# Optimization experiments

Hardware: AMD Instinct MI355X
Metric: run time of the kernel (lower is better)

The kernel has to match this reference:

```python
import jax, jax.numpy as jnp
import numpy as np

B = 1
DIM = 128
NUM_HEADS = 8
HEAD_DIM = DIM // NUM_HEADS
RES = (4, 16, 16, 16)            # (L, D, H, W)
FINE = (2, 8, 8, 8)
COARSE = (1, 2, 2, 2)
FINE_STRIDE = tuple(r // f for r, f in zip(RES, FINE))      # (2,2,2,2)
COARSE_STRIDE = tuple(r // c for r, c in zip(RES, COARSE))  # (4,8,8,8)
LOCAL = (1, 2, 2, 2)
HIDDEN = 512
SCALE = HEAD_DIM ** -0.5
EPS = 1e-5
_DN = jax.lax.ConvDimensionNumbers((0, 1, 2, 3, 4, 5), (0, 1, 2, 3, 4, 5), (0, 1, 2, 3, 4, 5))


def conv4d(x, w, b, stride=(1, 1, 1, 1)):
    # x: (B, L, C, D, H, W); channel axis is 2 (matches repo Conv4d usage). 'same'-style k//2 pad.
    xc = jnp.transpose(x, (0, 2, 1, 3, 4, 5))  # B,C,L,D,H,W
    pads = [(k // 2, k // 2) for k in w.shape[2:]]
    y = jax.lax.conv_general_dilated(xc, w, window_strides=stride, padding=pads, dimension_numbers=_DN)
    y = y + b[None, :, None, None, None, None]
    return jnp.transpose(y, (0, 2, 1, 3, 4, 5))


def layernorm(x, w, b):
    mu = jnp.mean(x, -1, keepdims=True)
    var = jnp.mean(jnp.square(x - mu), -1, keepdims=True)
    return (x - mu) * jax.lax.rsqrt(var + EPS) * w + b


def cnorm(x, w, b):
    # LayerNorm over channel axis (axis 2) of (B,L,C,D,H,W)
    xt = jnp.transpose(x, (0, 1, 3, 4, 5, 2))
    xt = layernorm(xt, w, b)
    return jnp.transpose(xt, (0, 1, 5, 2, 3, 4))


def to_tokens(t):
    # (B,L,C,D,H,W) -> (B, L*D*H*W, C)
    b, c = t.shape[0], t.shape[2]
    return jnp.swapaxes(jnp.transpose(t, (0, 2, 1, 3, 4, 5)).reshape(b, c, -1), 1, 2)


def split_heads(t):
    b, n, c = t.shape
    return jnp.transpose(t.reshape(b, n, NUM_HEADS, c // NUM_HEADS), (0, 2, 1, 3))


def slg(x, q_w, q_b, k_w, k_b, v_w, v_b, p_w, p_b, f_w, f_b, c_w, c_b, ln_w, ln_b):
    Bx, L, C, D, H, W = x.shape
    N = L * D * H * W
    q = split_heads(to_tokens(conv4d(x, q_w, q_b)))          # (B,h,N,hd)
    xc = conv4d(x, c_w, c_b, COARSE_STRIDE)                  # coarse pyramid (B,1,C,2,2,2)
    xf = conv4d(x, f_w, f_b, FINE_STRIDE)                    # fine pyramid   (B,2,C,8,8,8)
    kc = to_tokens(conv4d(xc, k_w, k_b))
    kf = to_tokens(conv4d(xf, k_w, k_b))
    vc = to_tokens(conv4d(xc, v_w, v_b))
    vf = to_tokens(conv4d(xf, v_w, v_b))
    k = split_heads(layernorm(jnp.concatenate([kc, kf], 1), ln_w, ln_b))
    v = split_heads(layernorm(jnp.concatenate([vc, vf], 1), ln_w, ln_b))
    attn = jax.nn.softmax(jnp.einsum('bhqd,bhkd->bhqk', q, k) * SCALE, axis=-1)
    y = jnp.einsum('bhqk,bhkd->bhqd', attn, v)               # (B,h,N,hd)
    y = jnp.transpose(y, (0, 2, 1, 3)).reshape(Bx, N, C)
    y = jnp.swapaxes(jnp.swapaxes(y, 1, 2).reshape(Bx, C, L, D, H, W), 1, 2)
    return conv4d(y, p_w, p_b)


def _win(t):
    # (B,Lh,C,D,H,W) -> (B, n_windows, heads, win_tokens, hd)
    b, l, c, d, h, w = t.shape
    ll, ld, lh, lw = LOCAL
    nl, nd, nh, nw = l // ll, d // ld, h // lh, w // lw
    t = jnp.transpose(t, (0, 2, 1, 3, 4, 5)).reshape(b, c, nl, ll, nd, ld, nh, lh, nw, lw)
    t = jnp.transpose(t, (0, 2, 4, 6, 8, 3, 5, 7, 9, 1))
    t = t.reshape(b, nl * nd * nh * nw, ll * ld * lh * lw, NUM_HEADS, c // NUM_HEADS)
    return jnp.transpose(t, (0, 1, 3, 2, 4))


def _unwin(y, shape):
    b, l, c, d, h, w = shape
    ll, ld, lh, lw = LOCAL
    nl, nd, nh, nw = l // ll, d // ld, h // lh, w // lw
    y = jnp.transpose(y, (0, 1, 3, 2, 4)).reshape(b, nl, nd, nh, nw, ll, ld, lh, lw, c)
    y = jnp.transpose(y, (0, 9, 1, 5, 2, 6, 3, 7, 4, 8)).reshape(b, c, l, d, h, w)
    return jnp.swapaxes(y, 1, 2)


def tlg(x, q_w, q_b, k_w, k_b, v_w, v_b, p_w, p_b):
    # stage < 2: first temporal half cross-attends with second half (windowed)
    L = x.shape[1]
    xs, xe = x[:, :L // 2], x[:, L // 2:]

    def cross(xq, xkv):
        q = _win(conv4d(xq, q_w, q_b))
        k = _win(conv4d(xkv, k_w, k_b))
        v = _win(conv4d(xkv, v_w, v_b))
        a = jax.nn.softmax(jnp.einsum('bnhqd,bnhkd->bnhqk', q, k) * SCALE, axis=-1)
        y = _unwin(jnp.einsum('bnhqk,bnhkd->bnhqd', a, v), xq.shape)
        return conv4d(y, p_w, p_b)

    return jnp.concatenate([cross(xs, xe), cross(xe, xs)], axis=1)


def _forward(x, n1_w, n1_b, tq_w, tq_b, tk_w, tk_b, tv_w, tv_b, tp_w, tp_b,
             n2_w, n2_b, sq_w, sq_b, sk_w, sk_b, sv_w, sv_b, sp_w, sp_b,
             sf_w, sf_b, sc_w, sc_b, sn_w, sn_b,
             n3_w, n3_b, m1_w, m1_b, m2_w, m2_b):
    x = x + tlg(cnorm(x, n1_w, n1_b), tq_w, tq_b, tk_w, tk_b, tv_w, tv_b, tp_w, tp_b)
    x = x + slg(cnorm(x, n2_w, n2_b), sq_w, sq_b, sk_w, sk_b, sv_w, sv_b, sp_w, sp_b,
                sf_w, sf_b, sc_w, sc_b, sn_w, sn_b)
    x = x + conv4d(jax.nn.relu(conv4d(cnorm(x, n3_w, n3_b), m1_w, m1_b)), m2_w, m2_b)
    return x


def setup_inputs():
    keys = iter(jax.random.split(jax.random.key(0), 64))

    def rn(shape, s=0.02):
        return jax.random.normal(next(keys), shape, dtype=jnp.float32) * s

    L, D, H, W = RES
    inp = {"x": jax.random.normal(next(keys), (B, L, DIM, D, H, W), dtype=jnp.float32)}
    for n in ("n1", "n2", "n3", "sn"):
        inp[n + "_w"] = jnp.ones((DIM,), jnp.float32)
        inp[n + "_b"] = jnp.zeros((DIM,), jnp.float32)
    for n in ("tq", "tk", "tv", "tp"):
        inp[n + "_w"] = rn((DIM, DIM, 3, 1, 1, 1))
        inp[n + "_b"] = jnp.zeros((DIM,), jnp.float32)
    for n in ("sq", "sk", "sv", "sp", "sf", "sc"):
        inp[n + "_w"] = rn((DIM, DIM, 1, 3, 3, 3))
        inp[n + "_b"] = jnp.zeros((DIM,), jnp.float32)
    inp["m1_w"] = rn((HIDDEN, DIM, 3, 3, 3, 3))
    inp["m1_b"] = jnp.zeros((HIDDEN,), jnp.float32)
    inp["m2_w"] = rn((DIM, HIDDEN, 3, 3, 3, 3))
    inp["m2_b"] = jnp.zeros((DIM,), jnp.float32)
    return inp


def reference(x, n1_w, n1_b, n2_w, n2_b, n3_w, n3_b, sn_w, sn_b,
              tq_w, tq_b, tk_w, tk_b, tv_w, tv_b, tp_w, tp_b,
              sq_w, sq_b, sk_w, sk_b, sv_w, sv_b, sp_w, sp_b,
              sf_w, sf_b, sc_w, sc_b, m1_w, m1_b, m2_w, m2_b):
    return _forward(x, n1_w, n1_b, tq_w, tq_b, tk_w, tk_b, tv_w, tv_b, tp_w, tp_b,
                    n2_w, n2_b, sq_w, sq_b, sk_w, sk_b, sv_w, sv_b, sp_w, sp_b,
                    sf_w, sf_b, sc_w, sc_b, sn_w, sn_b,
                    n3_w, n3_b, m1_w, m1_b, m2_w, m2_b)
```

## Files before the change

### kernel.cpp

```cpp
#include <hip/hip_runtime.h>

typedef unsigned short u16;
typedef __attribute__((ext_vector_type(8))) short bf16x8;
typedef __attribute__((ext_vector_type(4))) float f32x4;

#define PITCH 40

__device__ __forceinline__ u16 f2bf(float f) {
  union { float f; unsigned u; } v; v.f = f;
  unsigned r = v.u + 0x7fffu + ((v.u >> 16) & 1u);
  return (u16)(r >> 16);
}
__device__ __forceinline__ float bf2f(u16 h) {
  union { unsigned u; float f; } v; v.u = ((unsigned)h) << 16;
  return v.f;
}
__device__ __forceinline__ float4 load4bf(const u16* p) {
  ushort4 h = *(const ushort4*)p;
  return make_float4(bf2f(h.x), bf2f(h.y), bf2f(h.z), bf2f(h.w));
}
__device__ __forceinline__ void gll16(const u16* g, u16* l) {
  __builtin_amdgcn_global_load_lds(
      (const __attribute__((address_space(1))) unsigned int*)g,
      (__attribute__((address_space(3))) unsigned int*)l, 16, 0, 0);
}

__global__ __launch_bounds__(256) void k_tin(const float* __restrict__ x,
                                             float* __restrict__ xt) {
  __shared__ float t[32][33];
  int s0 = blockIdx.x * 32, c0 = blockIdx.y * 32, l = blockIdx.z;
  int r = threadIdx.x >> 3, q4 = (threadIdx.x & 7) * 4;
  float4 v = *(const float4*)(x + ((long)(l * 128 + c0 + r) << 12) + s0 + q4);
  t[r][q4] = v.x; t[r][q4 + 1] = v.y; t[r][q4 + 2] = v.z; t[r][q4 + 3] = v.w;
  __syncthreads();
  float4 o = {t[q4][r], t[q4 + 1][r], t[q4 + 2][r], t[q4 + 3][r]};
  *(float4*)(xt + ((long)(l * 4096 + s0 + r) << 7) + c0 + q4) = o;
}

__global__ __launch_bounds__(256) void k_tout(const float* __restrict__ xt,
                                              float* __restrict__ out) {
  __shared__ float t[32][33];
  int s0 = blockIdx.x * 32, c0 = blockIdx.y * 32, l = blockIdx.z;
  int r = threadIdx.x >> 3, q4 = (threadIdx.x & 7) * 4;
  float4 v = *(const float4*)(xt + ((long)(l * 4096 + s0 + r) << 7) + c0 + q4);
  t[r][q4] = v.x; t[r][q4 + 1] = v.y; t[r][q4 + 2] = v.z; t[r][q4 + 3] = v.w;
  __syncthreads();
  float4 o = {t[q4][r], t[q4 + 1][r], t[q4 + 2][r], t[q4 + 3][r]};
  *(float4*)(out + ((long)(l * 128 + c0 + r) << 12) + s0 + q4) = o;
}

__global__ __launch_bounds__(256) void k_zeropage(u16* __restrict__ zp) {
  zp[threadIdx.x] = 0; zp[threadIdx.x + 256] = 0;
  zp[threadIdx.x + 512] = 0; zp[threadIdx.x + 768] = 0;
}

__global__ __launch_bounds__(256) void k_ln_f2b(const float* __restrict__ X,
                                                const float* __restrict__ g,
                                                const float* __restrict__ b,
                                                u16* __restrict__ Y, int M,
                                                u16* __restrict__ Y2, int M1) {
  int n = blockIdx.x * 4 + (threadIdx.x >> 6);
  if (n >= M) return;
  int lane = threadIdx.x & 63;
  const float* row = X + (long)n * 128;
  float2 v = *(const float2*)(row + lane * 2);
  float s = v.x + v.y;
#pragma unroll
  for (int o = 32; o > 0; o >>= 1) s += __shfl_xor(s, o);
  float mu = s * (1.0f / 128.0f);
  float dx = v.x - mu, dy = v.y - mu;
  float q = dx * dx + dy * dy;
#pragma unroll
  for (int o = 32; o > 0; o >>= 1) q += __shfl_xor(q, o);
  float rs = rsqrtf(q * (1.0f / 128.0f) + 1e-5f);
  float2 gv = *(const float2*)(g + lane * 2);
  float2 bv = *(const float2*)(b + lane * 2);
  ushort2 o2;
  o2.x = f2bf(dx * rs * gv.x + bv.x);
  o2.y = f2bf(dy * rs * gv.y + bv.y);
  u16* yp = (n < M1) ? Y + (long)n * 128 : Y2 + (long)(n - M1) * 128;
  *(ushort2*)(yp + lane * 2) = o2;
}

__global__ __launch_bounds__(256) void k_repack2(const float* __restrict__ W,
                                                 u16* __restrict__ Wb,
                                                 int OC, int IC, int NT) {
  __shared__ float ws[128 * 81];
  int oc = blockIdx.x, ic0 = blockIdx.y * 128;
  const float* src = W + ((long)oc * IC + ic0) * NT;
  int n = 128 * NT;
  for (int i = threadIdx.x; i < n; i += 256) ws[i] = src[i];
  __syncthreads();
  u16* dst = Wb + (long)oc * IC + ic0;
  long tstep = (long)OC * IC;
  for (int idx = threadIdx.x; idx < n; idx += 256) {
    int t = idx >> 7, i = idx & 127;
    dst[(long)t * tstep + i] = f2bf(ws[i * NT + t]);
  }
}

struct RPargs { const float* w[6]; u16* wb[6]; };
__global__ __launch_bounds__(256) void k_repack_multi(RPargs a, int NT) {
  __shared__ float ws[128 * 27];
  int oc = blockIdx.x, slot = blockIdx.z;
  const int IC = 128;
  const float* src = a.w[slot] + (long)oc * IC * NT;
  int n = IC * NT;
  for (int i = threadIdx.x; i < n; i += 256) ws[i] = src[i];
  __syncthreads();
  u16* dst = a.wb[slot] + (long)oc * IC;
  long tstep = (long)128 * IC;
  for (int idx = threadIdx.x; idx < n; idx += 256) {
    int t = idx >> 7, i = idx & 127;
    dst[(long)t * tstep + i] = f2bf(ws[i * NT + t]);
  }
}

__global__ __launch_bounds__(256) void k_conv_mfma(
    const u16* __restrict__ X, const u16* __restrict__ W3,
    const float* __restrict__ bias, void* __restrict__ Yv,
    int M, int IC, int OC, int mode, int NT,
    int lgWo, int lgHo, int lgDo,
    int lgWi, int lgHi, int lgDi,
    int Li, int Di, int Hi, int Wi,
    int sL, int sD, int sH, int sW, int flags,
    long wgs, long ygs, const float* __restrict__ biasB) {
  __shared__ u16 As[64 * PITCH];
  __shared__ u16 Bs[64 * PITCH];
  int tid = threadIdx.x;
  int wave = tid >> 6, lane = tid & 63;
  int quad = lane >> 4, l15 = lane & 15;
  int m0 = blockIdx.x * 64;
  int oc0 = blockIdx.y * 64;
  int grp = blockIdx.z;
  W3 += (long)grp * wgs;
  if (grp) { bias = biasB; Yv = (void*)((float*)Yv + (long)grp * ygs); }

  int srl = tid >> 2;
  int sao = (tid & 3) * 8;
  int sboc = tid >> 2, sbo = (tid & 3) * 8;

  int sm = m0 + srl;
  bool mv = sm < M;
  int w = sm & ((1 << lgWo) - 1);
  int h = (sm >> lgWo) & ((1 << lgHo) - 1);
  int d = (sm >> (lgWo + lgHo)) & ((1 << lgDo) - 1);
  int l = sm >> (lgWo + lgHo + lgDo);

  int c0 = 0, c1 = 0, c2 = 0, c3 = 0;
  auto comp_nb = [&]() -> long {
    if (!mv) return -1;
    int li, di, hi, wi; bool ok;
    if (mode == 0) {
      int dl = c0 - 1;
      int ll = (l & 1) + dl;
      ok = (ll >= 0 && ll < 2);
      li = l + dl; di = d; hi = h; wi = w;
    } else if (mode == 1) {
      li = l * sL; di = d * sD + c2 - 1; hi = h * sH + c1 - 1; wi = w * sW + c0 - 1;
      ok = ((unsigned)di < (unsigned)Di) && ((unsigned)hi < (unsigned)Hi) &&
           ((unsigned)wi < (unsigned)Wi);
    } else {
      li = l + c3 - 1; di = d + c2 - 1; hi = h + c1 - 1; wi = w + c0 - 1;
      ok = ((unsigned)li < (unsigned)Li) && ((unsigned)di < (unsigned)Di) &&
           ((unsigned)hi < (unsigned)Hi) && ((unsigned)wi < (unsigned)Wi);
    }
    if (!ok) return -1;
    return ((((long)((li << lgDi) + di) << lgHi) + hi) << lgWi) + wi;
  };

  long nb = comp_nb();
  const u16* wt = W3 + (long)(oc0 + sboc) * IC + sbo;
  long wstep = (long)OC * IC;
  int kmask = (IC >> 5) - 1;
  int total = NT * (IC >> 5);

  const bf16x8 Z = {0, 0, 0, 0, 0, 0, 0, 0};
  bf16x8 ra0 = Z, rb;
  if (nb >= 0) ra0 = *(const bf16x8*)(X + nb * IC + sao);
  rb = *(const bf16x8*)wt;

  f32x4 acc[4];
#pragma unroll
  for (int j = 0; j < 4; ++j) acc[j] = {0.f, 0.f, 0.f, 0.f};

  int wrow = wave * 16;

  for (int ks = 0; ks < total; ++ks) {
    __syncthreads();
    *(bf16x8*)&As[srl * PITCH + sao] = ra0;
    *(bf16x8*)&Bs[sboc * PITCH + sbo] = rb;
    __syncthreads();
    int ksn = ks + 1;
    if (ksn < total) {
      int k0n = (ksn & kmask) << 5;
      if ((ksn & kmask) == 0) {
        wt += wstep;
        if (++c0 == 3) { c0 = 0; if (++c1 == 3) { c1 = 0; if (++c2 == 3) { c2 = 0; ++c3; } } }
        nb = comp_nb();
      }
      ra0 = Z;
      if (nb >= 0) ra0 = *(const bf16x8*)(X + nb * IC + k0n + sao);
      rb = *(const bf16x8*)(wt + k0n);
    }
    bf16x8 a0 = *(const bf16x8*)&As[(wrow + l15) * PITCH + quad * 8];
#pragma unroll
    for (int j = 0; j < 4; ++j) {
      bf16x8 b = *(const bf16x8*)&Bs[(j * 16 + l15) * PITCH + quad * 8];
      acc[j] = __builtin_amdgcn_mfma_f32_16x16x32_bf16(a0, b, acc[j], 0, 0, 0);
    }
  }

  int col = oc0 + l15;
#pragma unroll
  for (int j = 0; j < 4; ++j) {
    float bj = bias[col + j * 16];
    int rbase = m0 + wrow + quad * 4;
#pragma unroll
    for (int r = 0; r < 4; ++r) {
      int row = rbase + r;
      if (row >= M) continue;
      float v = acc[j][r] + bj;
      if (flags & 2) v = fmaxf(v, 0.f);
      long off = (long)row * OC + col + j * 16;
      if (flags & 4) ((u16*)Yv)[off] = f2bf(v);
      else if (flags & 1) ((float*)Yv)[off] += v;
      else ((float*)Yv)[off] = v;
    }
  }
}

__global__ __launch_bounds__(256, 4) void k_conv_gl(
    const u16* __restrict__ X, const u16* __restrict__ W3,
    const float* __restrict__ bias, void* __restrict__ Yv, float* __restrict__ SP,
    const u16* __restrict__ ZP,
    int M, int IC, int OC, int mode, int NT, int NSPLIT, long wgs,
    int lgWo, int lgHo, int lgDo,
    int lgWi, int lgHi, int lgDi,
    int Li, int Di, int Hi, int Wi,
    int sL, int sD, int sH, int sW, int flags) {
  __shared__ __align__(16) u16 As[128 * 64];
  __shared__ __align__(16) u16 Bs[128 * 64];
  int tid = threadIdx.x;
  int wave = tid >> 6, lane = tid & 63;
  int quad = lane >> 4, l15 = lane & 15;
  int m0 = blockIdx.x * 128, oc0 = blockIdx.y * 128;
  int mi = wave & 1, ni = wave >> 1;
  int zz = blockIdx.z;
  int grp = zz / NSPLIT, split = zz % NSPLIT;
  W3 += (long)grp * wgs;

  int rp[4], cA[4], sm[4];
#pragma unroll
  for (int q = 0; q < 4; ++q) {
    rp[q] = wave * 32 + q * 8 + (lane >> 3);
    cA[q] = ((lane & 7) - (rp[q] >> 1)) & 7;
    sm[q] = m0 + rp[q];
  }

  int tap_per = (NT + NSPLIT - 1) / NSPLIT;
  int t0 = split * tap_per;
  int t1 = min(NT, t0 + tap_per);
  int kc = IC >> 6;
  int total = (t1 - t0) * kc;

  int c0 = t0 % 3, c1 = (t0 / 3) % 3, c2 = (t0 / 9) % 3, c3 = t0 / 27;
  auto comp_nb = [&](int smv) -> int {
    if (smv >= M) return -1;
    int w = smv & ((1 << lgWo) - 1);
    int h = (smv >> lgWo) & ((1 << lgHo) - 1);
    int d = (smv >> (lgWo + lgHo)) & ((1 << lgDo) - 1);
    int l = smv >> (lgWo + lgHo + lgDo);
    int li, di, hi, wi; bool ok;
    if (mode == 0) {
      int dl = c0 - 1;
      int ll = (l & 1) + dl;
      ok = (ll >= 0 && ll < 2);
      li = l + dl; di = d; hi = h; wi = w;
    } else if (mode == 1) {
      li = l * sL; di = d * sD + c2 - 1; hi = h * sH + c1 - 1; wi = w * sW + c0 - 1;
      ok = ((unsigned)di < (unsigned)Di) && ((unsigned)hi < (unsigned)Hi) &&
           ((unsigned)wi < (unsigned)Wi);
    } else {
      li = l + c3 - 1; di = d + c2 - 1; hi = h + c1 - 1; wi = w + c0 - 1;
      ok = ((unsigned)li < (unsigned)Li) && ((unsigned)di < (unsigned)Di) &&
           ((unsigned)hi < (unsigned)Hi) && ((unsigned)wi < (unsigned)Wi);
    }
    if (!ok) return -1;
    return (((li << lgDi) + di) << lgHi | hi) << lgWi | wi;
  };

  int nb[4];
#pragma unroll
  for (int q = 0; q < 4; ++q) nb[q] = comp_nb(sm[q]);
  long wstep = (long)OC * IC;
  const u16* wbase = W3 + (long)t0 * wstep + (long)oc0 * IC;

  f32x4 acc[4][4];
#pragma unroll
  for (int i = 0; i < 4; ++i)
#pragma unroll
    for (int j = 0; j < 4; ++j) acc[i][j] = {0.f, 0.f, 0.f, 0.f};

  int kk = 0;
  for (int ks = 0; ks < total; ++ks) {
    if (kk == kc) {
      kk = 0;
// ... 245 lines not shown
    __builtin_amdgcn_sched_barrier(0);
    __builtin_amdgcn_s_barrier();
    mf(0);
    __builtin_amdgcn_s_barrier();
    rdA(rg + 1, 1);
    stageB();
    __builtin_amdgcn_sched_barrier(0);
    __builtin_amdgcn_s_barrier();
    mf(1);
    __builtin_amdgcn_sched_barrier(0);
    asm volatile("s_waitcnt vmcnt(8)" ::: "memory");
    __builtin_amdgcn_s_barrier();
  }

  if (NSPLIT > 1) {
    float* outp = SP + (long)blockIdx.z * M * OC;
#pragma unroll
    for (int i = 0; i < 8; ++i)
#pragma unroll
      for (int j = 0; j < 4; ++j) {
        int c = oc0 + (wc << 6) + (j << 4) + l15;
        int rb = m0 + (wr << 7) + (i << 4) + (quad << 2);
#pragma unroll
        for (int r = 0; r < 4; ++r) {
          int row = rb + r;
          if (row < M) outp[(long)row * OC + c] = acc[i][j][r];
        }
      }
  } else {
#pragma unroll
    for (int i = 0; i < 8; ++i)
#pragma unroll
      for (int j = 0; j < 4; ++j) {
        int c = oc0 + (wc << 6) + (j << 4) + l15;
        float bj = bias[c];
        int rb = m0 + (wr << 7) + (i << 4) + (quad << 2);
#pragma unroll
        for (int r = 0; r < 4; ++r) {
          int row = rb + r;
          if (row >= M) continue;
          float v = acc[i][j][r] + bj;
          if (flags & 2) v = fmaxf(v, 0.f);
          long off = (long)row * OC + c;
          if (flags & 4) ((u16*)Yv)[off] = f2bf(v);
          else if (flags & 1) ((float*)Yv)[off] += v;
          else ((float*)Yv)[off] = v;
        }
      }
  }
}

__global__ __launch_bounds__(256) void k_combine(const float* __restrict__ SP,
                                                 const float* __restrict__ bias,
                                                 void* __restrict__ out,
                                                 long MOC, int lgOC, int nsplit, int flags) {
  long idx = (long)blockIdx.x * 256 + threadIdx.x;
  if (idx >= MOC) return;
  float v = bias[idx & ((1 << lgOC) - 1)];
  for (int s = 0; s < nsplit; ++s) v += SP[s * MOC + idx];
  if (flags & 2) v = fmaxf(v, 0.f);
  if (flags & 4) ((u16*)out)[idx] = f2bf(v);
  else if (flags & 1) ((float*)out)[idx] += v;
  else ((float*)out)[idx] = v;
}

__global__ __launch_bounds__(256) void k_combine3(const float* __restrict__ SP,
                                                  const float* __restrict__ b0,
                                                  const float* __restrict__ b1,
                                                  const float* __restrict__ b2,
                                                  u16* __restrict__ out,
                                                  int lgMOC, int lgOC, int nsplit, int ngrp) {
  long idx = (long)blockIdx.x * 256 + threadIdx.x;
  long tot = (long)ngrp << lgMOC;
  if (idx >= tot) return;
  int grp = (int)(idx >> lgMOC);
  long sub = idx & ((1L << lgMOC) - 1);
  const float* bp = (grp == 0) ? b0 : ((grp == 1) ? b1 : b2);
  float v = bp[sub & ((1 << lgOC) - 1)];
  const float* sp = SP + (((long)grp * nsplit) << lgMOC);
  for (int s = 0; s < nsplit; ++s) v += sp[((long)s << lgMOC) + sub];
  out[idx] = f2bf(v);
}

__global__ __launch_bounds__(256) void k_tlg_attn(const u16* __restrict__ Q,
                                                  const u16* __restrict__ K,
                                                  const u16* __restrict__ V,
                                                  u16* __restrict__ Y) {
  int gw = blockIdx.x * 4 + (threadIdx.x >> 6);
  int lane = threadIdx.x & 63;
  int head = gw & 7;
  int win = gw >> 3;
  int wB = win & 7, hB = (win >> 3) & 7, dB = (win >> 6) & 7, l = win >> 9;
  int i = lane >> 3, j = lane & 7;
  int nq = (l << 12) | ((dB * 2 + (i >> 2)) << 8) | ((hB * 2 + ((i >> 1) & 1)) << 4) |
           (wB * 2 + (i & 1));
  int lk = l ^ 2;
  int nk = (lk << 12) | ((dB * 2 + (j >> 2)) << 8) | ((hB * 2 + ((j >> 1) & 1)) << 4) |
           (wB * 2 + (j & 1));
  int hoff = head * 16;
  const u16* qp = Q + (long)nq * 128 + hoff;
  const u16* kp = K + (long)nk * 128 + hoff;
  float s = 0.f;
#pragma unroll
  for (int t = 0; t < 16; t += 4) {
    float4 a = load4bf(qp + t);
    float4 b = load4bf(kp + t);
    s += a.x * b.x + a.y * b.y + a.z * b.z + a.w * b.w;
  }
  s *= 0.25f;
  float mx = s;
#pragma unroll
  for (int o = 1; o < 8; o <<= 1) mx = fmaxf(mx, __shfl_xor(mx, o));
  float e = __expf(s - mx);
  float sum = e;
#pragma unroll
  for (int o = 1; o < 8; o <<= 1) sum += __shfl_xor(sum, o);
  float p = e / sum;
  const u16* vp = V + (long)nk * 128 + hoff;
  float y[16];
#pragma unroll
  for (int t = 0; t < 16; t += 4) {
    float4 vv = load4bf(vp + t);
    y[t] = p * vv.x; y[t + 1] = p * vv.y; y[t + 2] = p * vv.z; y[t + 3] = p * vv.w;
  }
#pragma unroll
  for (int o = 1; o < 8; o <<= 1) {
#pragma unroll
    for (int t = 0; t < 16; ++t) y[t] += __shfl_xor(y[t], o);
  }
  if (j == 0) {
    u16* yp = Y + (long)nq * 128 + hoff;
    u16 tmp[16];
#pragma unroll
    for (int t = 0; t < 16; ++t) tmp[t] = f2bf(y[t]);
    *(uint4*)(yp) = *(uint4*)tmp;
    *(uint4*)(yp + 8) = *(uint4*)(tmp + 8);
  }
}

__global__ __launch_bounds__(256) void k_pack_kv(const u16* __restrict__ Kin,
                                                 const u16* __restrict__ Vin,
                                                 u16* __restrict__ Kh,
                                                 u16* __restrict__ Vt) {
  int idx = blockIdx.x * 256 + threadIdx.x;
  if (idx < 8 * 1032 * 16) {
    int d = idx & 15;
    int r = idx >> 4;
    int k = r % 1032, h = r / 1032;
    Kh[idx] = Kin[k * 128 + h * 16 + d];
  } else {
    int j = idx - 8 * 1032 * 16;
    int k = j % 1032;
    int r = j / 1032;
    int d = r & 15, h = r >> 4;
    Vt[j] = Vin[k * 128 + h * 16 + d];
  }
}

__global__ __launch_bounds__(256) void k_slg_flash(const u16* __restrict__ Q,
                                                   const u16* __restrict__ Kh,
                                                   const u16* __restrict__ Vt,
                                                   u16* __restrict__ Y) {
  constexpr int NK = 1032;
  constexpr int NTILE = 17;
  __shared__ __align__(16) u16 Ks[64 * 24];
  __shared__ __align__(16) u16 Vs[16 * 72];
  __shared__ __align__(16) u16 Ps[4][16 * 72];
  int tid = threadIdx.x;
  int wave = tid >> 6, lane = tid & 63;
  int quad = lane >> 4, l15 = lane & 15;
  int h = blockIdx.x & 7;
  int q0 = (blockIdx.x >> 3) * 64 + wave * 16;

  const bf16x8 Zb = {0, 0, 0, 0, 0, 0, 0, 0};
  bf16x8 qf = Zb;
  if (quad < 2) qf = *(const bf16x8*)(Q + (long)(q0 + l15) * 128 + h * 16 + quad * 8);

  const u16* Kbase = Kh + (long)h * NK * 16;
  const u16* Vbase = Vt + (long)h * 16 * NK;

  float mrow[4], lrow[4];
  f32x4 oacc = {0.f, 0.f, 0.f, 0.f};
#pragma unroll
  for (int r = 0; r < 4; ++r) { mrow[r] = -1e30f; lrow[r] = 0.f; }

  int skey = tid >> 2, sch = (tid & 3) * 4;
  int svd = tid >> 4, svc = (tid & 15) * 4;

  for (int t = 0; t < NTILE; ++t) {
    int k0 = t * 64;
    __syncthreads();
    {
      short4 v = {0, 0, 0, 0};
      int key = k0 + skey;
      if (key < NK) v = *(const short4*)(Kbase + key * 16 + sch);
      *(short4*)&Ks[skey * 24 + sch] = v;
    }
    {
      short4 v = {0, 0, 0, 0};
      int colb = k0 + svc;
      if (colb < NK) v = *(const short4*)(Vbase + svd * NK + colb);
      *(short4*)&Vs[svd * 72 + svc] = v;
    }
    __syncthreads();

    f32x4 s[4];
#pragma unroll
    for (int sub = 0; sub < 4; ++sub) {
      bf16x8 b = Zb;
      if (quad < 2) b = *(const bf16x8*)&Ks[(sub * 16 + l15) * 24 + quad * 8];
      f32x4 zero = {0.f, 0.f, 0.f, 0.f};
      s[sub] = __builtin_amdgcn_mfma_f32_16x16x32_bf16(qf, b, zero, 0, 0, 0);
    }
    float pv[4][4];
    float tmax[4] = {-1e30f, -1e30f, -1e30f, -1e30f};
#pragma unroll
    for (int sub = 0; sub < 4; ++sub) {
      int key = k0 + sub * 16 + l15;
      bool valid = key < NK;
#pragma unroll
      for (int r = 0; r < 4; ++r) {
        float sv = valid ? s[sub][r] * 0.25f : -1e30f;
        pv[sub][r] = sv;
        tmax[r] = fmaxf(tmax[r], sv);
      }
    }
#pragma unroll
    for (int o = 1; o < 16; o <<= 1)
#pragma unroll
      for (int r = 0; r < 4; ++r) tmax[r] = fmaxf(tmax[r], __shfl_xor(tmax[r], o));

    float al[4], tsum[4] = {0.f, 0.f, 0.f, 0.f};
#pragma unroll
    for (int r = 0; r < 4; ++r) {
      float mn = fmaxf(mrow[r], tmax[r]);
      al[r] = __expf(mrow[r] - mn);
      mrow[r] = mn;
    }
#pragma unroll
    for (int sub = 0; sub < 4; ++sub)
#pragma unroll
      for (int r = 0; r < 4; ++r) {
        float pe = __expf(pv[sub][r] - mrow[r]);
        tsum[r] += pe;
        Ps[wave][(quad * 4 + r) * 72 + sub * 16 + l15] = f2bf(pe);
      }
#pragma unroll
    for (int o = 1; o < 16; o <<= 1)
#pragma unroll
      for (int r = 0; r < 4; ++r) tsum[r] += __shfl_xor(tsum[r], o);
#pragma unroll
    for (int r = 0; r < 4; ++r) {
      lrow[r] = lrow[r] * al[r] + tsum[r];
      oacc[r] *= al[r];
    }
    bf16x8 pa0 = *(const bf16x8*)&Ps[wave][l15 * 72 + quad * 8];
    bf16x8 pa1 = *(const bf16x8*)&Ps[wave][l15 * 72 + 32 + quad * 8];
    bf16x8 vb0 = *(const bf16x8*)&Vs[l15 * 72 + quad * 8];
    bf16x8 vb1 = *(const bf16x8*)&Vs[l15 * 72 + 32 + quad * 8];
    oacc = __builtin_amdgcn_mfma_f32_16x16x32_bf16(pa0, vb0, oacc, 0, 0, 0);
    oacc = __builtin_amdgcn_mfma_f32_16x16x32_bf16(pa1, vb1, oacc, 0, 0, 0);
  }

#pragma unroll
  for (int r = 0; r < 4; ++r) {
    float inv = 1.0f / lrow[r];
    Y[(long)(q0 + quad * 4 + r) * 128 + h * 16 + l15] = f2bf(oacc[r] * inv);
  }
}

static inline int ilg(int v) { int r = 0; while ((1 << r) < v) ++r; return r; }

extern "C" void kernel_launch(void* const* d_in, const int* in_sizes, int n_in,
                              void* d_out, int out_size, void* d_ws, size_t ws_size,
                              hipStream_t stream) {
  (void)in_sizes; (void)n_in; (void)out_size; (void)ws_size;
  const float* x    = (const float*)d_in[0];
  const float* n1_w = (const float*)d_in[1];  const float* n1_b = (const float*)d_in[2];
  const float* n2_w = (const float*)d_in[3];  const float* n2_b = (const float*)d_in[4];
  const float* n3_w = (const float*)d_in[5];  const float* n3_b = (const float*)d_in[6];
  const float* sn_w = (const float*)d_in[7];  const float* sn_b = (const float*)d_in[8];
  const float* tq_w = (const float*)d_in[9];  const float* tq_b = (const float*)d_in[10];
  const float* tk_w = (const float*)d_in[11]; const float* tk_b = (const float*)d_in[12];
  const float* tv_w = (const float*)d_in[13]; const float* tv_b = (const float*)d_in[14];
  const float* tp_w = (const float*)d_in[15]; const float* tp_b = (const float*)d_in[16];
  const float* sq_w = (const float*)d_in[17]; const float* sq_b = (const float*)d_in[18];
  const float* sk_w = (const float*)d_in[19]; const float* sk_b = (const float*)d_in[20];
  const float* sv_w = (const float*)d_in[21]; const float* sv_b = (const float*)d_in[22];
  const float* sp_w = (const float*)d_in[23]; const float* sp_b = (const float*)d_in[24];
  const float* sf_w = (const float*)d_in[25]; const float* sf_b = (const float*)d_in[26];
  const float* sc_w = (const float*)d_in[27]; const float* sc_b = (const float*)d_in[28];
  const float* m1_w = (const float*)d_in[29]; const float* m1_b = (const float*)d_in[30];
  const float* m2_w = (const float*)d_in[31]; const float* m2_b = (const float*)d_in[32];

  char* p = (char*)d_ws;
  auto alloc = [&](size_t bytes) { char* r = p; p += (bytes + 255) & ~(size_t)255; return r; };
  const long N = 16384;
  float* X0 = (float*)alloc(N * 128 * 4);
  u16* XN = (u16*)alloc(N * 128 * 2);
  u16* Qb = (u16*)alloc(N * 128 * 2);
  u16* Kb = (u16*)alloc(N * 128 * 2);
  u16* Vb = (u16*)alloc(N * 128 * 2);
  u16* Yb = (u16*)alloc(N * 128 * 2);
  u16* H  = (u16*)alloc(N * 512 * 2);
  u16* XC = (u16*)alloc(8 * 128 * 2);
  u16* XF = (u16*)alloc(1024 * 128 * 2);
  float* Kf = (float*)alloc(1032 * 128 * 4);
  float* Vf = (float*)alloc(1032 * 128 * 4);
  u16* Kh = (u16*)alloc(8 * 1032 * 16 * 2);
  u16* Vt = (u16*)alloc(8 * 16 * 1032 * 2);
  float* SPb = (float*)alloc(2L * N * 512 * 4);
  u16* ZPb = (u16*)alloc(2048);
  u16* tq2 = (u16*)alloc(49152 * 2);  u16* tk2 = (u16*)alloc(49152 * 2);
  u16* tv2 = (u16*)alloc(49152 * 2);  u16* tp2 = (u16*)alloc(49152 * 2);
  u16* sq2 = (u16*)alloc(442368 * 2); u16* sk2 = (u16*)alloc(442368 * 2);
  u16* sv2 = (u16*)alloc(442368 * 2); u16* sp2 = (u16*)alloc(442368 * 2);
  u16* sf2 = (u16*)alloc(442368 * 2); u16* sc2 = (u16*)alloc(442368 * 2);
  u16* m12 = (u16*)alloc(5308416L * 2);
  u16* m22 = (u16*)alloc(5308416L * 2);

  k_zeropage<<<1, 256, 0, stream>>>(ZPb);

  {
    RPargs r1 = {{tq_w, tk_w, tv_w, tp_w, nullptr, nullptr},
                 {tq2, tk2, tv2, tp2, nullptr, nullptr}};
    k_repack_multi<<<dim3(128, 1, 4), 256, 0, stream>>>(r1, 3);
    RPargs r2 = {{sq_w, sk_w, sv_w, sp_w, sf_w, sc_w},
                 {sq2, sk2, sv2, sp2, sf2, sc2}};
    k_repack_multi<<<dim3(128, 1, 6), 256, 0, stream>>>(r2, 27);
    k_repack2<<<dim3(512, 1), 256, 0, stream>>>(m1_w, m12, 512, 128, 81);
    k_repack2<<<dim3(128, 4), 256, 0, stream>>>(m2_w, m22, 128, 512, 81);
  }

  auto conv = [&](const u16* Xp, const u16* Wp, const float* Bp, void* Yp,
                  int M, int IC, int OC, int mode, int NT,
                  int Do, int Ho, int Wo, int Li, int Di, int Hi, int Wi,
                  int sL, int sD, int sH, int sW, int flags,
                  int ngrp, long wgs, long ygs, const float* BpB) {
    int lgWo = ilg(Wo), lgHo = ilg(Ho), lgDo = ilg(Do);
    int lgWi = ilg(Wi), lgHi = ilg(Hi), lgDi = ilg(Di);
    dim3 g((M + 63) / 64, OC / 64, ngrp);
    k_conv_mfma<<<g, 256, 0, stream>>>(Xp, Wp, Bp, Yp, M, IC, OC, mode, NT,
                                       lgWo, lgHo, lgDo, lgWi, lgHi, lgDi,
                                       Li, Di, Hi, Wi, sL, sD, sH, sW, flags,
                                       wgs, ygs, BpB);
  };
  auto conv_gl = [&](const u16* Xp, const u16* Wp, const float* Bp, void* Yp,
                     int M, int IC, int OC, int mode, int NT, int nsplit, int flags) {
    dim3 g(M / 128, OC / 128, nsplit);
    k_conv_gl<<<g, 256, 0, stream>>>(Xp, Wp, Bp, Yp, SPb, ZPb, M, IC, OC, mode, NT, nsplit,
                                     0L, 4, 4, 4, 4, 4, 4, 4, 16, 16, 16, 1, 1, 1, 1, flags);
    if (nsplit > 1) {
      long MOC = (long)M * OC;
      k_combine<<<(int)((MOC + 255) / 256), 256, 0, stream>>>(SPb, Bp, Yp, MOC, ilg(OC),
                                                              nsplit, flags);
    }
  };
  auto conv_gl256 = [&](const u16* Xp, const u16* Wp, const float* Bp, void* Yp,
                        int M, int IC, int OC, int mode, int NT, int nsplit, int flags) {
    dim3 g(M / 256, OC / 256, nsplit);
    k_conv_g256<<<g, 512, 0, stream>>>(Xp, Wp, Bp, Yp, SPb, ZPb, M, IC, OC, mode, NT, nsplit,
                                       4, 4, 4, 4, 4, 4, 4, 16, 16, 16, 1, 1, 1, 1, flags);
    if (nsplit > 1) {
      long MOC = (long)M * OC;
      k_combine<<<(int)((MOC + 255) / 256), 256, 0, stream>>>(SPb, Bp, Yp, MOC, ilg(OC),
                                                              nsplit, flags);
    }
  };

  k_tin<<<dim3(128, 4, 4), 256, 0, stream>>>(x, X0);

  k_ln_f2b<<<4096, 256, 0, stream>>>(X0, n1_w, n1_b, XN, 16384, XN, 16384);
  {
    dim3 g(128, 1, 6);
    k_conv_gl<<<g, 256, 0, stream>>>(XN, tq2, tq_b, Qb, SPb, ZPb, 16384, 128, 128, 0, 3, 2,
                                     49152L, 4, 4, 4, 4, 4, 4, 4, 16, 16, 16, 1, 1, 1, 1, 4);
    k_combine3<<<24576, 256, 0, stream>>>(SPb, tq_b, tk_b, tv_b, Qb, 21, 7, 2, 3);
  }
  k_tlg_attn<<<4096, 256, 0, stream>>>(Qb, Kb, Vb, Yb);
  conv_gl(Yb, tp2, tp_b, X0, 16384, 128, 128, 0, 3, 3, 1);

  k_ln_f2b<<<4096, 256, 0, stream>>>(X0, n2_w, n2_b, XN, 16384, XN, 16384);
  conv_gl(XN, sq2, sq_b, Qb, 16384, 128, 128, 1, 27, 7, 4);
  conv(XN, sc2, sc_b, XC, 8,    128, 128, 1, 27, 2, 2, 2, 4, 16, 16, 16, 4, 8, 8, 8, 4,
       1, 0L, 0L, sc_b);
  conv(XN, sf2, sf_b, XF, 1024, 128, 128, 1, 27, 8, 8, 8, 4, 16, 16, 16, 2, 2, 2, 2, 4,
       1, 0L, 0L, sf_b);
  conv(XC, sk2, sk_b, Kf, 8, 128, 128, 1, 27, 2, 2, 2, 1, 2, 2, 2, 1, 1, 1, 1, 0,
       2, 442368L, (long)1032 * 128, sv_b);
  conv(XF, sk2, sk_b, Kf + 8 * 128, 1024, 128, 128, 1, 27, 8, 8, 8, 2, 8, 8, 8, 1, 1, 1, 1, 0,
       2, 442368L, (long)1032 * 128, sv_b);
  k_ln_f2b<<<516, 256, 0, stream>>>(Kf, sn_w, sn_b, Kb, 2064, Vb, 1032);
  k_pack_kv<<<1032, 256, 0, stream>>>(Kb, Vb, Kh, Vt);
  k_slg_flash<<<2048, 256, 0, stream>>>(Qb, Kh, Vt, Yb);
  conv_gl(Yb, sp2, sp_b, X0, 16384, 128, 128, 1, 27, 7, 1);

  k_ln_f2b<<<4096, 256, 0, stream>>>(X0, n3_w, n3_b, XN, 16384, XN, 16384);
  conv_gl256(XN, m12, m1_b, H, 16384, 128, 512, 2, 81, 2, 6);
  conv_gl(H, m22, m2_b, X0, 16384, 512, 128, 2, 81, 8, 1);

  k_tout<<<dim3(128, 4, 4), 256, 0, stream>>>(X0, (float*)d_out);
}
```

Measured before the change: 1.019 ms.

## Fuse transpose, layernorm, split-K combine and KV pack into fewer kernels

Merges the input transpose with the first layernorm, folds each split-K combine and residual add into the following layernorm or the output transpose, and fuses the KV layernorm with the head pack. The small coarse/fine and K/V convolutions are batched into grouped launches, and all weight repacks plus the zero page go into one kernel. The aim is to cut launch count and intermediate global-memory round trips. In exchange the conv kernel is specialised to 128 channels and 27 taps, which drops its generality.

After: 877.7 us. -13.8%, faster.

```diff
diff --git a/kernel.cpp b/kernel.cpp
--- a/kernel.cpp
+++ b/kernel.cpp
@@ -25,45 +25,7 @@
       (__attribute__((address_space(3))) unsigned int*)l, 16, 0, 0);
 }
 
-__global__ __launch_bounds__(256) void k_tin(const float* __restrict__ x,
-                                             float* __restrict__ xt) {
-  __shared__ float t[32][33];
-  int s0 = blockIdx.x * 32, c0 = blockIdx.y * 32, l = blockIdx.z;
-  int r = threadIdx.x >> 3, q4 = (threadIdx.x & 7) * 4;
-  float4 v = *(const float4*)(x + ((long)(l * 128 + c0 + r) << 12) + s0 + q4);
-  t[r][q4] = v.x; t[r][q4 + 1] = v.y; t[r][q4 + 2] = v.z; t[r][q4 + 3] = v.w;
-  __syncthreads();
-  float4 o = {t[q4][r], t[q4 + 1][r], t[q4 + 2][r], t[q4 + 3][r]};
-  *(float4*)(xt + ((long)(l * 4096 + s0 + r) << 7) + c0 + q4) = o;
-}
-
-__global__ __launch_bounds__(256) void k_tout(const float* __restrict__ xt,
-                                              float* __restrict__ out) {
-  __shared__ float t[32][33];
-  int s0 = blockIdx.x * 32, c0 = blockIdx.y * 32, l = blockIdx.z;
-  int r = threadIdx.x >> 3, q4 = (threadIdx.x & 7) * 4;
-  float4 v = *(const float4*)(xt + ((long)(l * 4096 + s0 + r) << 7) + c0 + q4);
-  t[r][q4] = v.x; t[r][q4 + 1] = v.y; t[r][q4 + 2] = v.z; t[r][q4 + 3] = v.w;
-  __syncthreads();
-  float4 o = {t[q4][r], t[q4 + 1][r], t[q4 + 2][r], t[q4 + 3][r]};
-  *(float4*)(out + ((long)(l * 128 + c0 + r) << 12) + s0 + q4) = o;
-}
-
-__global__ __launch_bounds__(256) void k_zeropage(u16* __restrict__ zp) {
-  zp[threadIdx.x] = 0; zp[threadIdx.x + 256] = 0;
-  zp[threadIdx.x + 512] = 0; zp[threadIdx.x + 768] = 0;
-}
-
-__global__ __launch_bounds__(256) void k_ln_f2b(const float* __restrict__ X,
-                                                const float* __restrict__ g,
-                                                const float* __restrict__ b,
-                                                u16* __restrict__ Y, int M,
-                                                u16* __restrict__ Y2, int M1) {
-  int n = blockIdx.x * 4 + (threadIdx.x >> 6);
-  if (n >= M) return;
-  int lane = threadIdx.x & 63;
-  const float* row = X + (long)n * 128;
-  float2 v = *(const float2*)(row + lane * 2);
+__device__ __forceinline__ ushort2 ln_row(float2 v, float2 gv, float2 bv) {
   float s = v.x + v.y;
 #pragma unroll
   for (int o = 32; o > 0; o >>= 1) s += __shfl_xor(s, o);
@@ -73,68 +35,97 @@
 #pragma unroll
   for (int o = 32; o > 0; o >>= 1) q += __shfl_xor(q, o);
   float rs = rsqrtf(q * (1.0f / 128.0f) + 1e-5f);
-  float2 gv = *(const float2*)(g + lane * 2);
-  float2 bv = *(const float2*)(b + lane * 2);
   ushort2 o2;
   o2.x = f2bf(dx * rs * gv.x + bv.x);
   o2.y = f2bf(dy * rs * gv.y + bv.y);
-  u16* yp = (n < M1) ? Y + (long)n * 128 : Y2 + (long)(n - M1) * 128;
-  *(ushort2*)(yp + lane * 2) = o2;
-}
-
-__global__ __launch_bounds__(256) void k_repack2(const float* __restrict__ W,
-                                                 u16* __restrict__ Wb,
-                                                 int OC, int IC, int NT) {
+  return o2;
+}
+
+__global__ __launch_bounds__(256) void k_tin_ln(const float* __restrict__ x,
+                                                float* __restrict__ X0,
+                                                const float* __restrict__ g,
+                                                const float* __restrict__ b,
+                                                u16* __restrict__ XN) {
+  __shared__ float t[128][33];
+  int s0 = blockIdx.x * 32, l = blockIdx.y;
+  int tid = threadIdx.x;
+#pragma unroll
+  for (int r = 0; r < 4; ++r) {
+    int lin = r * 256 + tid;
+    int c = lin >> 3, sq = (lin & 7) * 4;
+    float4 v = *(const float4*)(x + ((long)(l * 128 + c) << 12) + s0 + sq);
+    t[c][sq] = v.x; t[c][sq + 1] = v.y; t[c][sq + 2] = v.z; t[c][sq + 3] = v.w;
+  }
+  __syncthreads();
+  int wave = tid >> 6, lane = tid & 63;
+  int c2 = lane * 2;
+  float2 gv = *(const float2*)(g + c2);
+  float2 bv = *(const float2*)(b + c2);
+#pragma unroll
+  for (int p = 0; p < 8; ++p) {
+    int s = p * 4 + wave;
+    float2 v = make_float2(t[c2][s], t[c2 + 1][s]);
+    long token = (long)l * 4096 + s0 + s;
+    *(float2*)(X0 + token * 128 + c2) = v;
+    ushort2 o2 = ln_row(v, gv, bv);
+    *(ushort2*)(XN + token * 128 + c2) = o2;
+  }
+}
+
+struct RAargs { const float* w[12]; u16* wb[12]; u16* zp; };
+__global__ __launch_bounds__(256) void k_repack_all(RAargs a) {
   __shared__ float ws[128 * 81];
-  int oc = blockIdx.x, ic0 = blockIdx.y * 128;
-  const float* src = W + ((long)oc * IC + ic0) * NT;
+  int z = blockIdx.z, x = blockIdx.x, tid = threadIdx.x;
+  if (z == 0 && x == 0) ((unsigned long long*)a.zp)[tid] = 0ull;
+  if (z < 10 && x >= 128) return;
+  int NT = (z < 4) ? 3 : ((z < 10) ? 27 : 81);
+  int OC = (z == 10) ? 512 : 128;
+  int IC = (z == 11) ? 512 : 128;
+  int oc, ic0;
+  if (z == 11) { oc = x & 127; ic0 = (x >> 7) << 7; }
+  else { oc = x; ic0 = 0; }
+  const float* src = a.w[z] + ((long)oc * IC + ic0) * NT;
   int n = 128 * NT;
-  for (int i = threadIdx.x; i < n; i += 256) ws[i] = src[i];
+  for (int i = tid; i < n; i += 256) ws[i] = src[i];
   __syncthreads();
-  u16* dst = Wb + (long)oc * IC + ic0;
+  u16* dst = a.wb[z] + (long)oc * IC + ic0;
   long tstep = (long)OC * IC;
-  for (int idx = threadIdx.x; idx < n; idx += 256) {
+  for (int idx = tid; idx < n; idx += 256) {
     int t = idx >> 7, i = idx & 127;
     dst[(long)t * tstep + i] = f2bf(ws[i * NT + t]);
   }
 }
 
-struct RPargs { const float* w[6]; u16* wb[6]; };
-__global__ __launch_bounds__(256) void k_repack_multi(RPargs a, int NT) {
-  __shared__ float ws[128 * 27];
-  int oc = blockIdx.x, slot = blockIdx.z;
-  const int IC = 128;
-  const float* src = a.w[slot] + (long)oc * IC * NT;
-  int n = IC * NT;
-  for (int i = threadIdx.x; i < n; i += 256) ws[i] = src[i];
-  __syncthreads();
-  u16* dst = a.wb[slot] + (long)oc * IC;
-  long tstep = (long)128 * IC;
-  for (int idx = threadIdx.x; idx < n; idx += 256) {
-    int t = idx >> 7, i = idx & 127;
-    dst[(long)t * tstep + i] = f2bf(ws[i * NT + t]);
-  }
-}
-
-__global__ __launch_bounds__(256) void k_conv_mfma(
-    const u16* __restrict__ X, const u16* __restrict__ W3,
-    const float* __restrict__ bias, void* __restrict__ Yv,
-    int M, int IC, int OC, int mode, int NT,
-    int lgWo, int lgHo, int lgDo,
-    int lgWi, int lgHi, int lgDi,
-    int Li, int Di, int Hi, int Wi,
-    int sL, int sD, int sH, int sW, int flags,
-    long wgs, long ygs, const float* __restrict__ biasB) {
+struct QC {
+  const u16* X[4]; const u16* W[4]; const float* B[4]; void* Y[4];
+  int M[4];
+  int lgo[4][3];
+  int lgi[4][3];
+  int di[4][3];
+  int st[4][4];
+  int flags[4];
+};
+__global__ __launch_bounds__(256) void k_conv_quad(QC a) {
   __shared__ u16 As[64 * PITCH];
   __shared__ u16 Bs[64 * PITCH];
+  int grp = blockIdx.z;
+  int M = a.M[grp];
+  int m0 = blockIdx.x * 64;
+  if (m0 >= M) return;
+  const u16* X = a.X[grp];
+  const u16* W3 = a.W[grp];
+  const float* bias = a.B[grp];
+  void* Yv = a.Y[grp];
+  int lgWo = a.lgo[grp][0], lgHo = a.lgo[grp][1], lgDo = a.lgo[grp][2];
+  int lgWi = a.lgi[grp][0], lgHi = a.lgi[grp][1], lgDi = a.lgi[grp][2];
+  int Di = a.di[grp][0], Hi = a.di[grp][1], Wi = a.di[grp][2];
+  int sL = a.st[grp][0], sD = a.st[grp][1], sH = a.st[grp][2], sW = a.st[grp][3];
+  int flags = a.flags[grp];
+
   int tid = threadIdx.x;
   int wave = tid >> 6, lane = tid & 63;
   int quad = lane >> 4, l15 = lane & 15;
-  int m0 = blockIdx.x * 64;
   int oc0 = blockIdx.y * 64;
-  int grp = blockIdx.z;
-  W3 += (long)grp * wgs;
-  if (grp) { bias = biasB; Yv = (void*)((float*)Yv + (long)grp * ygs); }
 
   int srl = tid >> 2;
   int sao = (tid & 3) * 8;
@@ -150,34 +141,23 @@
   int c0 = 0, c1 = 0, c2 = 0, c3 = 0;
   auto comp_nb = [&]() -> long {
     if (!mv) return -1;
-    int li, di, hi, wi; bool ok;
-    if (mode == 0) {
-      int dl = c0 - 1;
-      int ll = (l & 1) + dl;
-      ok = (ll >= 0 && ll < 2);
-      li = l + dl; di = d; hi = h; wi = w;
-    } else if (mode == 1) {
-      li = l * sL; di = d * sD + c2 - 1; hi = h * sH + c1 - 1; wi = w * sW + c0 - 1;
-      ok = ((unsigned)di < (unsigned)Di) && ((unsigned)hi < (unsigned)Hi) &&
-           ((unsigned)wi < (unsigned)Wi);
-    } else {
-      li = l + c3 - 1; di = d + c2 - 1; hi = h + c1 - 1; wi = w + c0 - 1;
-      ok = ((unsigned)li < (unsigned)Li) && ((unsigned)di < (unsigned)Di) &&
-           ((unsigned)hi < (unsigned)Hi) && ((unsigned)wi < (unsigned)Wi);
-    }
+    int li = l * sL, di = d * sD + c2 - 1, hi = h * sH + c1 - 1, wi = w * sW + c0 - 1;
+    bool ok = ((unsigned)di < (unsigned)Di) && ((unsigned)hi < (unsigned)Hi) &&
+              ((unsigned)wi < (unsigned)Wi);
+    (void)c3;
     if (!ok) return -1;
     return ((((long)((li << lgDi) + di) << lgHi) + hi) << lgWi) + wi;
   };
 
   long nb = comp_nb();
-  const u16* wt = W3 + (long)(oc0 + sboc) * IC + sbo;
-  long wstep = (long)OC * IC;
-  int kmask = (IC >> 5) - 1;
-  int total = NT * (IC >> 5);
+  const u16* wt = W3 + (long)(oc0 + sboc) * 128 + sbo;
+  const long wstep = 128 * 128;
+  const int kmask = 3;
+  const int total = 27 * 4;
 
   const bf16x8 Z = {0, 0, 0, 0, 0, 0, 0, 0};
   bf16x8 ra0 = Z, rb;
-  if (nb >= 0) ra0 = *(const bf16x8*)(X + nb * IC + sao);
+  if (nb >= 0) ra0 = *(const bf16x8*)(X + nb * 128 + sao);
   rb = *(const bf16x8*)wt;
 
   f32x4 acc[4];
@@ -200,7 +180,7 @@
         nb = comp_nb();
       }
       ra0 = Z;
-      if (nb >= 0) ra0 = *(const bf16x8*)(X + nb * IC + k0n + sao);
+      if (nb >= 0) ra0 = *(const bf16x8*)(X + nb * 128 + k0n + sao);
       rb = *(const bf16x8*)(wt + k0n);
     }
     bf16x8 a0 = *(const bf16x8*)&As[(wrow + l15) * PITCH + quad * 8];
@@ -222,7 +202,7 @@
       if (row >= M) continue;
       float v = acc[j][r] + bj;
       if (flags & 2) v = fmaxf(v, 0.f);
-      long off = (long)row * OC + col + j * 16;
+      long off = (long)row * 128 + col + j * 16;
       if (flags & 4) ((u16*)Yv)[off] = f2bf(v);
       else if (flags & 1) ((float*)Yv)[off] += v;
       else ((float*)Yv)[off] = v;
@@ -634,6 +614,52 @@
   out[idx] = f2bf(v);
 }
 
+__global__ __launch_bounds__(256) void k_comb_ln(const float* __restrict__ SP,
+                                                 const float* __restrict__ bias,
+                                                 float* __restrict__ X0,
+                                                 const float* __restrict__ g,
+                                                 const float* __restrict__ b,
+                                                 u16* __restrict__ XN, int nsplit) {
+  int n = blockIdx.x * 4 + (threadIdx.x >> 6);
+  int lane = threadIdx.x & 63;
+  long off = (long)n * 128 + lane * 2;
+  float2 v = *(const float2*)(bias + lane * 2);
+  for (int s = 0; s < nsplit; ++s) {
+    float2 sv = *(const float2*)(SP + (((long)s) << 21) + off);
+    v.x += sv.x; v.y += sv.y;
+  }
+  float2 x0 = *(const float2*)(X0 + off);
+  v.x += x0.x; v.y += x0.y;
+  *(float2*)(X0 + off) = v;
+  float2 gv = *(const float2*)(g + lane * 2);
+  float2 bv = *(const float2*)(b + lane * 2);
+  ushort2 o2 = ln_row(v, gv, bv);
+  *(ushort2*)(XN + off) = o2;
+}
+
+__global__ __launch_bounds__(256) void k_comb_out(const float* __restrict__ SP,
+                                                  const float* __restrict__ X0,
+                                                  const float* __restrict__ bias,
+                                                  float* __restrict__ out) {
+  __shared__ float t[32][33];
+  int s0 = blockIdx.x * 32, c0 = blockIdx.y * 32, l = blockIdx.z;
+  int r = threadIdx.x >> 3, q4 = (threadIdx.x & 7) * 4;
+  long token = (long)l * 4096 + s0 + r;
+  long off = token * 128 + c0 + q4;
+  float4 v = *(const float4*)(bias + c0 + q4);
+#pragma unroll
+  for (int s = 0; s < 8; ++s) {
+    float4 sv = *(const float4*)(SP + (((long)s) << 21) + off);
+    v.x += sv.x; v.y += sv.y; v.z += sv.z; v.w += sv.w;
+  }
+  float4 x0 = *(const float4*)(X0 + off);
+  v.x += x0.x; v.y += x0.y; v.z += x0.z; v.w += x0.w;
+  t[r][q4] = v.x; t[r][q4 + 1] = v.y; t[r][q4 + 2] = v.z; t[r][q4 + 3] = v.w;
+  __syncthreads();
+  float4 o = {t[q4][r], t[q4 + 1][r], t[q4 + 2][r], t[q4 + 3][r]};
+  *(float4*)(out + ((long)(l * 128 + c0 + r) << 12) + s0 + q4) = o;
+}
+
 __global__ __launch_bounds__(256) void k_tlg_attn(const u16* __restrict__ Q,
                                                   const u16* __restrict__ K,
                                                   const u16* __restrict__ V,
@@ -690,22 +716,26 @@
   }
 }
 
-__global__ __launch_bounds__(256) void k_pack_kv(const u16* __restrict__ Kin,
-                                                 const u16* __restrict__ Vin,
-                                                 u16* __restrict__ Kh,
-                                                 u16* __restrict__ Vt) {
-  int idx = blockIdx.x * 256 + threadIdx.x;
-  if (idx < 8 * 1032 * 16) {
-    int d = idx & 15;
-    int r = idx >> 4;
-    int k = r % 1032, h = r / 1032;
-    Kh[idx] = Kin[k * 128 + h * 16 + d];
+__global__ __launch_bounds__(256) void k_ln_kv(const float* __restrict__ X,
+                                               const float* __restrict__ g,
+                                               const float* __restrict__ b,
+                                               u16* __restrict__ Kh,
+                                               u16* __restrict__ Vt) {
+  int n = blockIdx.x * 4 + (threadIdx.x >> 6);
+  if (n >= 2064) return;
+  int lane = threadIdx.x & 63;
+  float2 v = *(const float2*)(X + (long)n * 128 + lane * 2);
+  float2 gv = *(const float2*)(g + lane * 2);
+  float2 bv = *(const float2*)(b + lane * 2);
+  ushort2 o2 = ln_row(v, gv, bv);
+  int isK = n < 1032;
+  int k = isK ? n : n - 1032;
+  int h = lane >> 3, d = (lane & 7) * 2;
+  if (isK) {
+    *(ushort2*)(Kh + (((long)h * 1032 + k) << 4) + d) = o2;
   } else {
-    int j = idx - 8 * 1032 * 16;
-    int k = j % 1032;
-    int r = j / 1032;
-    int d = r & 15, h = r >> 4;
-    Vt[j] = Vin[k * 128 + h * 16 + d];
+    Vt[((long)(h * 16 + d)) * 1032 + k] = o2.x;
+    Vt[((long)(h * 16 + d) + 1) * 1032 + k] = o2.y;
   }
 }
 
@@ -871,38 +901,22 @@
   u16* m12 = (u16*)alloc(5308416L * 2);
   u16* m22 = (u16*)alloc(5308416L * 2);
 
-  k_zeropage<<<1, 256, 0, stream>>>(ZPb);
-
   {
-    RPargs r1 = {{tq_w, tk_w, tv_w, tp_w, nullptr, nullptr},
-                 {tq2, tk2, tv2, tp2, nullptr, nullptr}};
-    k_repack_multi<<<dim3(128, 1, 4), 256, 0, stream>>>(r1, 3);
-    RPargs r2 = {{sq_w, sk_w, sv_w, sp_w, sf_w, sc_w},
-                 {sq2, sk2, sv2, sp2, sf2, sc2}};
-    k_repack_multi<<<dim3(128, 1, 6), 256, 0, stream>>>(r2, 27);
-    k_repack2<<<dim3(512, 1), 256, 0, stream>>>(m1_w, m12, 512, 128, 81);
-    k_repack2<<<dim3(128, 4), 256, 0, stream>>>(m2_w, m22, 128, 512, 81);
-  }
-
-  auto conv = [&](const u16* Xp, const u16* Wp, const float* Bp, void* Yp,
-                  int M, int IC, int OC, int mode, int NT,
-                  int Do, int Ho, int Wo, int Li, int Di, int Hi, int Wi,
-                  int sL, int sD, int sH, int sW, int flags,
-                  int ngrp, long wgs, long ygs, const float* BpB) {
-    int lgWo = ilg(Wo), lgHo = ilg(Ho), lgDo = ilg(Do);
-    int lgWi = ilg(Wi), lgHi = ilg(Hi), lgDi = ilg(Di);
-    dim3 g((M + 63) / 64, OC / 64, ngrp);
-    k_conv_mfma<<<g, 256, 0, stream>>>(Xp, Wp, Bp, Yp, M, IC, OC, mode, NT,
-                                       lgWo, lgHo, lgDo, lgWi, lgHi, lgDi,
-                                       Li, Di, Hi, Wi, sL, sD, sH, sW, flags,
-                                       wgs, ygs, BpB);
-  };
+    RAargs ra;
+    const float* ws[12] = {tq_w, tk_w, tv_w, tp_w, sq_w, sk_w, sv_w, sp_w, sf_w, sc_w,
+                           m1_w, m2_w};
+    u16* wbs[12] = {tq2, tk2, tv2, tp2, sq2, sk2, sv2, sp2, sf2, sc2, m12, m22};
+    for (int i = 0; i < 12; ++i) { ra.w[i] = ws[i]; ra.wb[i] = wbs[i]; }
+    ra.zp = ZPb;
+    k_repack_all<<<dim3(512, 1, 12), 256, 0, stream>>>(ra);
+  }
+
   auto conv_gl = [&](const u16* Xp, const u16* Wp, const float* Bp, void* Yp,
                      int M, int IC, int OC, int mode, int NT, int nsplit, int flags) {
     dim3 g(M / 128, OC / 128, nsplit);
     k_conv_gl<<<g, 256, 0, stream>>>(Xp, Wp, Bp, Yp, SPb, ZPb, M, IC, OC, mode, NT, nsplit,
                                      0L, 4, 4, 4, 4, 4, 4, 4, 16, 16, 16, 1, 1, 1, 1, flags);
-    if (nsplit > 1) {
+    if (nsplit > 1 && flags >= 0) {
       long MOC = (long)M * OC;
       k_combine<<<(int)((MOC + 255) / 256), 256, 0, stream>>>(SPb, Bp, Yp, MOC, ilg(OC),
                                                               nsplit, flags);
@@ -920,9 +934,8 @@
     }
   };
 
-  k_tin<<<dim3(128, 4, 4), 256, 0, stream>>>(x, X0);
-
-  k_ln_f2b<<<4096, 256, 0, stream>>>(X0, n1_w, n1_b, XN, 16384, XN, 16384);
+  k_tin_ln<<<dim3(128, 4), 256, 0, stream>>>(x, X0, n1_w, n1_b, XN);
+
   {
     dim3 g(128, 1, 6);
     k_conv_gl<<<g, 256, 0, stream>>>(XN, tq2, tq_b, Qb, SPb, ZPb, 16384, 128, 128, 0, 3, 2,
@@ -930,26 +943,64 @@
     k_combine3<<<24576, 256, 0, stream>>>(SPb, tq_b, tk_b, tv_b, Qb, 21, 7, 2, 3);
   }
   k_tlg_attn<<<4096, 256, 0, stream>>>(Qb, Kb, Vb, Yb);
-  conv_gl(Yb, tp2, tp_b, X0, 16384, 128, 128, 0, 3, 3, 1);
-
-  k_ln_f2b<<<4096, 256, 0, stream>>>(X0, n2_w, n2_b, XN, 16384, XN, 16384);
+  {
+    dim3 g(128, 1, 3);
+    k_conv_gl<<<g, 256, 0, stream>>>(Yb, tp2, tp_b, X0, SPb, ZPb, 16384, 128, 128, 0, 3, 3,
+                                     0L, 4, 4, 4, 4, 4, 4, 4, 16, 16, 16, 1, 1, 1, 1, 1);
+    k_comb_ln<<<4096, 256, 0, stream>>>(SPb, tp_b, X0, n2_w, n2_b, XN, 3);
+  }
+
   conv_gl(XN, sq2, sq_b, Qb, 16384, 128, 128, 1, 27, 7, 4);
-  conv(XN, sc2, sc_b, XC, 8,    128, 128, 1, 27, 2, 2, 2, 4, 16, 16, 16, 4, 8, 8, 8, 4,
-       1, 0L, 0L, sc_b);
-  conv(XN, sf2, sf_b, XF, 1024, 128, 128, 1, 27, 8, 8, 8, 4, 16, 16, 16, 2, 2, 2, 2, 4,
-       1, 0L, 0L, sf_b);
-  conv(XC, sk2, sk_b, Kf, 8, 128, 128, 1, 27, 2, 2, 2, 1, 2, 2, 2, 1, 1, 1, 1, 0,
-       2, 442368L, (long)1032 * 128, sv_b);
-  conv(XF, sk2, sk_b, Kf + 8 * 128, 1024, 128, 128, 1, 27, 8, 8, 8, 2, 8, 8, 8, 1, 1, 1, 1, 0,
-       2, 442368L, (long)1032 * 128, sv_b);
-  k_ln_f2b<<<516, 256, 0, stream>>>(Kf, sn_w, sn_b, Kb, 2064, Vb, 1032);
-  k_pack_kv<<<1032, 256, 0, stream>>>(Kb, Vb, Kh, Vt);
+  {
+    QC q{};
+    q.X[0] = XN; q.W[0] = sc2; q.B[0] = sc_b; q.Y[0] = XC; q.M[0] = 8;
+    q.lgo[0][0] = 1; q.lgo[0][1] = 1; q.lgo[0][2] = 1;
+    q.lgi[0][0] = 4; q.lgi[0][1] = 4; q.lgi[0][2] = 4;
+    q.di[0][0] = 16; q.di[0][1] = 16; q.di[0][2] = 16;
+    q.st[0][0] = 4; q.st[0][1] = 8; q.st[0][2] = 8; q.st[0][3] = 8;
+    q.flags[0] = 4;
+    q.X[1] = XN; q.W[1] = sf2; q.B[1] = sf_b; q.Y[1] = XF; q.M[1] = 1024;
+    q.lgo[1][0] = 3; q.lgo[1][1] = 3; q.lgo[1][2] = 3;
+    q.lgi[1][0] = 4; q.lgi[1][1] = 4; q.lgi[1][2] = 4;
+    q.di[1][0] = 16; q.di[1][1] = 16; q.di[1][2] = 16;
+    q.st[1][0] = 2; q.st[1][1] = 2; q.st[1][2] = 2; q.st[1][3] = 2;
+    q.flags[1] = 4;
+    k_conv_quad<<<dim3(16, 2, 2), 256, 0, stream>>>(q);
+  }
+  {
+    QC q{};
+    for (int i = 0; i < 4; ++i) {
+      int fine = i >> 1, isv = i & 1;
+      q.X[i] = fine ? XF : XC;
+      q.W[i] = isv ? sv2 : sk2;
+      q.B[i] = isv ? sv_b : sk_b;
+      q.Y[i] = (void*)((isv ? Vf : Kf) + (fine ? 8 * 128 : 0));
+      q.M[i] = fine ? 1024 : 8;
+      int lo = fine ? 3 : 1;
+      q.lgo[i][0] = lo; q.lgo[i][1] = lo; q.lgo[i][2] = lo;
+      int li = fine ? 3 : 1;
+      q.lgi[i][0] = li; q.lgi[i][1] = li; q.lgi[i][2] = li;
+      int dd = fine ? 8 : 2;
+      q.di[i][0] = dd; q.di[i][1] = dd; q.di[i][2] = dd;
+      q.st[i][0] = 1; q.st[i][1] = 1; q.st[i][2] = 1; q.st[i][3] = 1;
+      q.flags[i] = 0;
+    }
+    k_conv_quad<<<dim3(16, 2, 4), 256, 0, stream>>>(q);
+  }
+  k_ln_kv<<<516, 256, 0, stream>>>(Kf, sn_w, sn_b, Kh, Vt);
   k_slg_flash<<<2048, 256, 0, stream>>>(Qb, Kh, Vt, Yb);
-  conv_gl(Yb, sp2, sp_b, X0, 16384, 128, 128, 1, 27, 7, 1);
-
-  k_ln_f2b<<<4096, 256, 0, stream>>>(X0, n3_w, n3_b, XN, 16384, XN, 16384);
+  {
+    dim3 g(128, 1, 7);
+    k_conv_gl<<<g, 256, 0, stream>>>(Yb, sp2, sp_b, X0, SPb, ZPb, 16384, 128, 128, 1, 27, 7,
+                                     0L, 4, 4, 4, 4, 4, 4, 4, 16, 16, 16, 1, 1, 1, 1, 1);
+    k_comb_ln<<<4096, 256, 0, stream>>>(SPb, sp_b, X0, n3_w, n3_b, XN, 7);
+  }
+
   conv_gl256(XN, m12, m1_b, H, 16384, 128, 512, 2, 81, 2, 6);
-  conv_gl(H, m22, m2_b, X0, 16384, 512, 128, 2, 81, 8, 1);
-
-  k_tout<<<dim3(128, 4, 4), 256, 0, stream>>>(X0, (float*)d_out);
-}
+  {
+    dim3 g(128, 1, 8);
+    k_conv_gl<<<g, 256, 0, stream>>>(H, m22, m2_b, X0, SPb, ZPb, 16384, 512, 128, 2, 81, 8,
+                                     0L, 4, 4, 4, 4, 4, 4, 4, 16, 16, 16, 1, 1, 1, 1, 1);
+    k_comb_out<<<dim3(128, 4, 4), 256, 0, stream>>>(SPb, X0, m2_b, (float*)d_out);
+  }
+}
```
